# Performance work log

Hardware: AMD Instinct MI355X
Metric: run time of the kernel (lower is better)

The kernel has to match this reference:

```python
import jax, jax.numpy as jnp
import numpy as np

N, E, F_IN, H, C = 50000, 800000, 50, 128, 121


def setup_inputs() -> dict:
    key = jax.random.key(0)
    ks = jax.random.split(key, 16)
    s = 0.05
    inp = {
        'x': jax.random.normal(ks[0], (N, F_IN), jnp.float32),
        'edge_index': jax.random.randint(ks[1], (2, E), 0, N, jnp.int64),
        'TRAIN': 0,
        'W1': jax.random.normal(ks[2], (F_IN, H), jnp.float32) * s,
        'b1': jnp.zeros((H,), jnp.float32),
        'W2': jax.random.normal(ks[3], (H, H), jnp.float32) * s,
        'b2': jnp.zeros((H,), jnp.float32),
        'W3': jax.random.normal(ks[4], (H, H), jnp.float32) * s,
        'b3': jnp.zeros((H,), jnp.float32),
        'fcW1': jax.random.normal(ks[5], (H, H), jnp.float32) * s,
        'fcb1': jnp.zeros((H,), jnp.float32),
        'fcW2': jax.random.normal(ks[6], (H, H), jnp.float32) * s,
        'fcb2': jnp.zeros((H,), jnp.float32),
        'fcW3': jax.random.normal(ks[7], (H, C), jnp.float32) * s,
        'fcb3': jnp.zeros((C,), jnp.float32),
    }
    return inp


def gcn_conv(x, W, b, src, dst, n):
    # PyG GCNConv: h = x @ W; symmetric norm with self-loops; aggregate at dst.
    h = x @ W
    deg = jax.ops.segment_sum(jnp.ones(src.shape[0], h.dtype), dst, num_segments=n) + 1.0
    dinv = jax.lax.rsqrt(deg)  # deg^{-1/2}, self-loop included
    norm = dinv[src] * dinv[dst]  # [E]
    agg = jax.ops.segment_sum(h[src] * norm[:, None], dst, num_segments=n)
    agg = agg + h * (dinv * dinv)[:, None]  # self-loop contribution
    return agg + b


def reference(x, edge_index, TRAIN, W1, b1, W2, b2, W3, b3, fcW1, fcb1, fcW2, fcb2, fcW3, fcb3):
    src, dst = edge_index[0], edge_index[1]
    n = x.shape[0]
    y = jax.nn.relu(gcn_conv(x, W1, b1, src, dst, n))
    y = jax.nn.relu(gcn_conv(y, W2, b2, src, dst, n))
    y = jax.nn.relu(gcn_conv(y, W3, b3, src, dst, n))
    y = jax.nn.relu(y @ fcW1 + fcb1)
    y = jax.nn.relu(y @ fcW2 + fcb2)
    y = y @ fcW3 + fcb3
    return y
```

## Files before the change

### kernel.cpp

```cpp
#include <hip/hip_runtime.h>

#define SCAN_CHUNK 2048

typedef short s16x8 __attribute__((ext_vector_type(8)));
typedef float f32x4 __attribute__((ext_vector_type(4)));

__device__ inline ushort f2b(float f) {
  uint u = __float_as_uint(f);
  return (ushort)((u + 0x7fffu + ((u >> 16) & 1u)) >> 16);
}
__device__ inline float b2f(uint h) { return __uint_as_float(h << 16); }

__global__ __launch_bounds__(256) void convert_hist_kernel(const void* __restrict__ ei,
                                                           int* __restrict__ src,
                                                           int* __restrict__ dst,
                                                           int* __restrict__ degi, int E) {
  __shared__ int sflag;
  if (threadIdx.x == 0) {
    const int* p32 = (const int*)ei;
    int is64 = 1;
#pragma unroll 4
    for (int i = 1; i < 256; i += 2)
      if (p32[i] != 0) { is64 = 0; break; }
    sflag = is64;
  }
  __syncthreads();
  int e = blockIdx.x * 256 + threadIdx.x;
  if (e >= E) return;
  int s, d;
  if (sflag) {
    const long long* p = (const long long*)ei;
    s = (int)p[e];
    d = (int)p[E + e];
  } else {
    const int* p = (const int*)ei;
    s = p[e];
    d = p[E + e];
  }
  src[e] = s;
  dst[e] = d;
  atomicAdd(&degi[d], 1);
}

__global__ __launch_bounds__(256) void chunk_reduce_kernel(const int* __restrict__ degi,
                                                           int* __restrict__ partials, int N) {
  __shared__ int s[256];
  int base = blockIdx.x * SCAN_CHUNK;
  int sum = 0;
  for (int j = 0; j < 8; ++j) {
    int i = base + threadIdx.x * 8 + j;
    if (i < N) sum += degi[i];
  }
  s[threadIdx.x] = sum;
  __syncthreads();
  for (int ofs = 128; ofs > 0; ofs >>= 1) {
    if ((int)threadIdx.x < ofs) s[threadIdx.x] += s[threadIdx.x + ofs];
    __syncthreads();
  }
  if (threadIdx.x == 0) partials[blockIdx.x] = s[0];
}

__global__ __launch_bounds__(256) void chunk_scan_kernel(int* __restrict__ degi,
                                                         const int* __restrict__ partials,
                                                         int nchunk,
                                                         int* __restrict__ rowptr,
                                                         float* __restrict__ dinv,
                                                         int N, int E) {
  __shared__ int s[256];
  __shared__ int sbase;
  int t = threadIdx.x;
  if (t == 0) {
    int acc = 0;
    for (int c = 0; c < (int)blockIdx.x; ++c) acc += partials[c];
    sbase = acc;
    if (blockIdx.x == 0) rowptr[N] = E;
  }
  int base = blockIdx.x * SCAN_CHUNK;
  int v[8];
  int tsum = 0;
  for (int j = 0; j < 8; ++j) {
    int i = base + t * 8 + j;
    v[j] = (i < N) ? degi[i] : 0;
    tsum += v[j];
  }
  s[t] = tsum;
  __syncthreads();
  for (int ofs = 1; ofs < 256; ofs <<= 1) {
    int add = (t >= ofs) ? s[t - ofs] : 0;
    __syncthreads();
    s[t] += add;
    __syncthreads();
  }
  int run = s[t] - tsum + sbase;
  for (int j = 0; j < 8; ++j) {
    int i = base + t * 8 + j;
    if (i < N) {
      rowptr[i] = run;
      dinv[i] = rsqrtf((float)v[j] + 1.0f);
      degi[i] = 0;
    }
    run += v[j];
  }
}

__global__ __launch_bounds__(256) void scatter_kernel(const int* __restrict__ src,
                                                      const int* __restrict__ dst,
                                                      const int* __restrict__ rowptr,
                                                      const float* __restrict__ dinv,
                                                      int* __restrict__ cnt,
                                                      uint* __restrict__ epack, int E, int N) {
  const int chunk = blockIdx.x & 7;
  const int group = blockIdx.x >> 3;
  const int ngroup = gridDim.x >> 3;
  const int c0 = (int)(((long)chunk * N) >> 3);
  const int c1 = (int)(((long)(chunk + 1) * N) >> 3);
  for (int e = group * 256 + threadIdx.x; e < E; e += ngroup * 256) {
    int d = dst[e];
    if (d < c0 || d >= c1) continue;
    int s = src[e];
    int slot = rowptr[d] + atomicAdd(&cnt[d], 1);
    float nm = dinv[s] * dinv[d];
    epack[slot] = (uint)s | ((uint)f2b(nm) << 16);
  }
}

__global__ __launch_bounds__(256) void prep_all(const float* __restrict__ W1,
                                                const float* __restrict__ W2,
                                                const float* __restrict__ W3,
                                                const float* __restrict__ F1,
                                                const float* __restrict__ F2,
                                                const float* __restrict__ F3,
                                                const float* __restrict__ x,
                                                ushort* __restrict__ W1t, ushort* __restrict__ W2t,
                                                ushort* __restrict__ W3t, ushort* __restrict__ F1t,
                                                ushort* __restrict__ F2t, ushort* __restrict__ F3t,
                                                ushort* __restrict__ xb, int N) {
  int b = blockIdx.x;
  if (b < 384) {
    int wi = b >> 6;
    int i = (b & 63) * 256 + threadIdx.x;
    const float* W;
    ushort* Wt;
    int K, Kp, ncol;
    switch (wi) {
      case 0: W = W1; Wt = W1t; K = 50; Kp = 64; ncol = 128; break;
      case 1: W = W2; Wt = W2t; K = 128; Kp = 128; ncol = 128; break;
      case 2: W = W3; Wt = W3t; K = 128; Kp = 128; ncol = 128; break;
      case 3: W = F1; Wt = F1t; K = 128; Kp = 128; ncol = 128; break;
      case 4: W = F2; Wt = F2t; K = 128; Kp = 128; ncol = 128; break;
      default: W = F3; Wt = F3t; K = 128; Kp = 128; ncol = 121; break;
    }
    if (i >= 128 * Kp) return;
    int c = i / Kp, k = i - c * Kp;
    float w = (k < K && c < ncol) ? W[(size_t)k * ncol + c] : 0.f;
    ushort hi = f2b(w);
    float rem = w - b2f(hi);
    Wt[(size_t)c * Kp + k] = hi;
    Wt[(size_t)128 * Kp + (size_t)c * Kp + k] = f2b(rem);
  } else {
    long i = (long)(b - 384) * 256 + threadIdx.x;
    if (i >= (long)N * 64) return;
    int n = (int)(i >> 6), k = (int)(i & 63);
    xb[i] = (k < 50) ? f2b(x[(size_t)n * 50 + k]) : (ushort)0;
  }
}

template <int KSTEPS, bool BIAS, bool RELU>
__global__ __launch_bounds__(256) void mm_mfma(const ushort* __restrict__ X,
                                               const ushort* __restrict__ Wt,
                                               const float* __restrict__ bias,
                                               ushort* __restrict__ Yb, int N) {
  constexpr int K = KSTEPS * 32;
  const int lane = threadIdx.x & 63;
  const int wq = threadIdx.x >> 6;
  const long r0 = (long)blockIdx.x * 32;
  if (r0 >= N) return;
  const bool v1 = (r0 + 16) < N;
  const int am = lane & 15;
  const int ag = lane >> 4;
  const ushort* __restrict__ x0 = X + (size_t)(r0 + am) * K + ag * 8;

  f32x4 acc[2][2] = {};
  for (int ks = 0; ks < KSTEPS; ++ks) {
    s16x8 a0 = *(const s16x8*)(x0 + ks * 32);
    s16x8 a1 = {};
    if (v1) a1 = *(const s16x8*)(x0 + (size_t)16 * K + ks * 32);
#pragma unroll
    for (int f = 0; f < 2; ++f) {
      const ushort* wp = Wt + (size_t)(wq * 32 + f * 16 + am) * K + ag * 8 + ks * 32;
      s16x8 bh = *(const s16x8*)(wp);
      s16x8 bl = *(const s16x8*)(wp + (size_t)128 * K);
      acc[0][f] = __builtin_amdgcn_mfma_f32_16x16x32_bf16(a0, bh, acc[0][f], 0, 0, 0);
      acc[0][f] = __builtin_amdgcn_mfma_f32_16x16x32_bf16(a0, bl, acc[0][f], 0, 0, 0);
      if (v1) {
        acc[1][f] = __builtin_amdgcn_mfma_f32_16x16x32_bf16(a1, bh, acc[1][f], 0, 0, 0);
        acc[1][f] = __builtin_amdgcn_mfma_f32_16x16x32_bf16(a1, bl, acc[1][f], 0, 0, 0);
      }
    }
  }

  const int dr = ag * 4;
#pragma unroll
  for (int m = 0; m < 2; ++m) {
    if (m == 1 && !v1) break;
#pragma unroll
    for (int f = 0; f < 2; ++f) {
      int col = wq * 32 + f * 16 + am;
      float bv = BIAS ? bias[col] : 0.f;
#pragma unroll
      for (int r = 0; r < 4; ++r) {
        long row = r0 + m * 16 + dr + r;
        float v = acc[m][f][r] + bv;
        if (RELU) v = fmaxf(v, 0.f);
        Yb[row * 128 + col] = f2b(v);
      }
    }
  }
}

__global__ __launch_bounds__(256) void fc_fused(const ushort* __restrict__ X,
                                                const ushort* __restrict__ F1t,
                                                const ushort* __restrict__ F2t,
                                                const ushort* __restrict__ F3t,
                                                const float* __restrict__ b1,
                                                const float* __restrict__ b2,
                                                const float* __restrict__ b3,
                                                float* __restrict__ out, int N) {
  __shared__ ushort lds[32 * 128];
  const int lane = threadIdx.x & 63;
  const int wq = threadIdx.x >> 6;
  const long r0 = (long)blockIdx.x * 32;
  if (r0 >= N) return;
  const bool v1 = (r0 + 16) < N;
  const int am = lane & 15;
  const int ag = lane >> 4;
  char* my = (char*)lds;

  auto stage = [&](f32x4 acc[2][2], const float* __restrict__ bias) {
#pragma unroll
    for (int m = 0; m < 2; ++m)
#pragma unroll
      for (int f = 0; f < 2; ++f) {
        int col = wq * 32 + f * 16 + am;
        float bv = bias[col];
#pragma unroll
        for (int r = 0; r < 4; ++r) {
          int row = m * 16 + ag * 4 + r;
          uint byte = (uint)(row * 256 + col * 2) ^ ((uint)(row & 7) << 4);
          *(ushort*)(my + byte) = f2b(fmaxf(acc[m][f][r] + bv, 0.f));
        }
      }
  };
  auto loadA = [&](int m, int ks) -> s16x8 {
    int row = m * 16 + am;
    uint byte = (uint)(row * 256 + ks * 64 + ag * 16) ^ ((uint)(row & 7) << 4);
    return *(const s16x8*)(my + byte);
  };
  auto layer = [&](f32x4 acc[2][2], const ushort* __restrict__ Wt, bool fromLds,
                   const ushort* __restrict__ x0) {
#pragma unroll
    for (int ks = 0; ks < 4; ++ks) {
      s16x8 a0, a1;
      if (fromLds) {
        a0 = loadA(0, ks);
        a1 = loadA(1, ks);
      } else {
        a0 = *(const s16x8*)(x0 + ks * 32);
        a1 = v1 ? *(const s16x8*)(x0 + (size_t)16 * 128 + ks * 32) : s16x8{};
      }
#pragma unroll
      for (int f = 0; f < 2; ++f) {
        const ushort* wp = Wt + (size_t)(wq * 32 + f * 16 + am) * 128 + ag * 8 + ks * 32;
        s16x8 bh = *(const s16x8*)(wp);
        s16x8 bl = *(const s16x8*)(wp + (size_t)128 * 128);
        acc[0][f] = __builtin_amdgcn_mfma_f32_16x16x32_bf16(a0, bh, acc[0][f], 0, 0, 0);
        acc[0][f] = __builtin_amdgcn_mfma_f32_16x16x32_bf16(a0, bl, acc[0][f], 0, 0, 0);
        acc[1][f] = __builtin_amdgcn_mfma_f32_16x16x32_bf16(a1, bh, acc[1][f], 0, 0, 0);
        acc[1][f] = __builtin_amdgcn_mfma_f32_16x16x32_bf16(a1, bl, acc[1][f], 0, 0, 0);
      }
    }
  };

  const ushort* x0 = X + (size_t)(r0 + am) * 128 + ag * 8;
  f32x4 a1c[2][2] = {};
  layer(a1c, F1t, false, x0);
  stage(a1c, b1);
  __syncthreads();
  f32x4 a2c[2][2] = {};
  layer(a2c, F2t, true, nullptr);
  __syncthreads();
  stage(a2c, b2);
  __syncthreads();
  f32x4 a3c[2][2] = {};
  layer(a3c, F3t, true, nullptr);

#pragma unroll
  for (int m = 0; m < 2; ++m) {
    if (m == 1 && !v1) break;
#pragma unroll
    for (int f = 0; f < 2; ++f) {
      int col = wq * 32 + f * 16 + am;
      if (col >= 121) continue;
      float bv = b3[col];
#pragma unroll
      for (int r = 0; r < 4; ++r) {
        long row = r0 + m * 16 + ag * 4 + r;
        if (row < N) out[row * 121 + col] = a3c[m][f][r] + bv;
      }
    }
  }
}

template <int RW, bool ACT>
__global__ __launch_bounds__(256) void agg_kernel(const ushort* __restrict__ Hm,
                                                  const int* __restrict__ rowptr,
                                                  const uint* __restrict__ epack,
                                                  const float* __restrict__ dinv,
                                                  const float* __restrict__ b,
                                                  ushort* __restrict__ Y, int N) {
  int wave = threadIdx.x >> 6;
  int lane = threadIdx.x & 63;
  int n = blockIdx.x * 4 + wave;
  if (n >= N) return;
  int beg = rowptr[n], end = rowptr[n + 1];
  float dn = dinv[n];
  float d2 = dn * dn;
  int i = beg;

  if constexpr (RW == 128) {
    int f = lane * 2;
    float ax = 0.f, ay = 0.f;
    while (i + 8 <= end) {
      uint rec[8];
#pragma unroll
      for (int j = 0; j < 8; ++j) rec[j] = epack[i + j];
      uint v[8];
#pragma unroll
      for (int j = 0; j < 8; ++j)
        v[j] = *(const uint*)&Hm[(size_t)(rec[j] & 0xffffu) * 128 + f];
#pragma unroll
      for (int j = 0; j < 8; ++j) {
        float nm = __uint_as_float(rec[j] & 0xffff0000u);
        ax += b2f(v[j] & 0xffffu) * nm;
        ay += b2f(v[j] >> 16) * nm;
      }
      i += 8;
    }
    if (i + 4 <= end) {
      uint rec[4];
#pragma unroll
      for (int j = 0; j < 4; ++j) rec[j] = epack[i + j];
      uint v[4];
#pragma unroll
      for (int j = 0; j < 4; ++j)
        v[j] = *(const uint*)&Hm[(size_t)(rec[j] & 0xffffu) * 128 + f];
#pragma unroll
      for (int j = 0; j < 4; ++j) {
        float nm = __uint_as_float(rec[j] & 0xffff0000u);
        ax += b2f(v[j] & 0xffffu) * nm;
        ay += b2f(v[j] >> 16) * nm;
      }
      i += 4;
    }
    for (; i < end; ++i) {
      uint rec = epack[i];
      float nm = __uint_as_float(rec & 0xffff0000u);
      uint v = *(const uint*)&Hm[(size_t)(rec & 0xffffu) * 128 + f];
      ax += b2f(v & 0xffffu) * nm;
      ay += b2f(v >> 16) * nm;
    }
    uint sv = *(const uint*)&Hm[(size_t)n * 128 + f];
    ax += b2f(sv & 0xffffu) * d2;
    ay += b2f(sv >> 16) * d2;
    if (ACT) {
      ax = fmaxf(ax + b[f], 0.f);
      ay = fmaxf(ay + b[f + 1], 0.f);
    }
    uint out = (uint)f2b(ax) | ((uint)f2b(ay) << 16);
    *(uint*)&Y[(size_t)n * 128 + f] = out;
  } else {
    int f = lane;
    float ax = 0.f;
    while (i + 8 <= end) {
      uint rec[8];
#pragma unroll
      for (int j = 0; j < 8; ++j) rec[j] = epack[i + j];
      ushort v[8];
#pragma unroll
      for (int j = 0; j < 8; ++j)
        v[j] = Hm[(size_t)(rec[j] & 0xffffu) * 64 + f];
#pragma unroll
      for (int j = 0; j < 8; ++j)
        ax += b2f(v[j]) * __uint_as_float(rec[j] & 0xffff0000u);
      i += 8;
    }
    if (i + 4 <= end) {
      uint rec[4];
#pragma unroll
      for (int j = 0; j < 4; ++j) rec[j] = epack[i + j];
      ushort v[4];
#pragma unroll
      for (int j = 0; j < 4; ++j)
        v[j] = Hm[(size_t)(rec[j] & 0xffffu) * 64 + f];
#pragma unroll
      for (int j = 0; j < 4; ++j)
        ax += b2f(v[j]) * __uint_as_float(rec[j] & 0xffff0000u);
      i += 4;
    }
    for (; i < end; ++i) {
      uint rec = epack[i];
      ax += b2f(Hm[(size_t)(rec & 0xffffu) * 64 + f]) * __uint_as_float(rec & 0xffff0000u);
    }
    ax += b2f(Hm[(size_t)n * 64 + f]) * d2;
    if (ACT) ax = fmaxf(ax + b[f], 0.f);
    Y[(size_t)n * 64 + f] = f2b(ax);
  }
}

extern "C" void kernel_launch(void* const* d_in, const int* in_sizes, int n_in,
                              void* d_out, int out_size, void* d_ws, size_t ws_size,
                              hipStream_t stream) {
  const float* x    = (const float*)d_in[0];
  const void*  ei   = d_in[1];
  const float* W1   = (const float*)d_in[3];
  const float* b1   = (const float*)d_in[4];
  const float* W2   = (const float*)d_in[5];
  const float* b2   = (const float*)d_in[6];
  const float* W3   = (const float*)d_in[7];
  const float* b3   = (const float*)d_in[8];
  const float* fcW1 = (const float*)d_in[9];
  const float* fcb1 = (const float*)d_in[10];
  const float* fcW2 = (const float*)d_in[11];
  const float* fcb2 = (const float*)d_in[12];
  const float* fcW3 = (const float*)d_in[13];
  const float* fcb3 = (const float*)d_in[14];

  const int FIN = 50;
  const int N = in_sizes[0] / FIN;
  const int E = in_sizes[1] / 2;
  const int NCHUNK = (N + SCAN_CHUNK - 1) / SCAN_CHUNK;

  size_t off = 0;
  auto carve = [&](size_t bytes) {
    void* p = (char*)d_ws + off;
    off += (bytes + 255) & ~(size_t)255;
    return p;
  };
  int*    src32    = (int*)carve((size_t)E * 4);
  int*    dst32    = (int*)carve((size_t)E * 4);
  uint*   epack    = (uint*)carve((size_t)E * 4);
  int*    degi     = (int*)carve((size_t)N * 4);
  int*    rowptr   = (int*)carve((size_t)(N + 1) * 4);
  float*  dinv     = (float*)carve((size_t)N * 4);
  int*    partials = (int*)carve((size_t)NCHUNK * 4);
  ushort* W1t      = (ushort*)carve((size_t)2 * 128 * 64 * 2);
  ushort* W2t      = (ushort*)carve((size_t)2 * 128 * 128 * 2);
  ushort* W3t      = (ushort*)carve((size_t)2 * 128 * 128 * 2);
  ushort* F1t      = (ushort*)carve((size_t)2 * 128 * 128 * 2);
  ushort* F2t      = (ushort*)carve((size_t)2 * 128 * 128 * 2);
  ushort* F3t      = (ushort*)carve((size_t)2 * 128 * 128 * 2);
  ushort* xb       = (ushort*)carve((size_t)N * 64 * 2);
  ushort* aggX     = (ushort*)carve((size_t)N * 64 * 2);
  ushort* bufA     = (ushort*)carve((size_t)N * 128 * 2);
  ushort* bufB     = (ushort*)carve((size_t)N * 128 * 2);

  const int gE = (E + 255) / 256;
  const int gMM = (N + 31) / 32;
  const int gAGG = (N + 3) / 4;
  const int gPREP = 384 + (int)(((long)N * 64 + 255) / 256);

  hipMemsetAsync(degi, 0, (size_t)N * 4, stream);
  convert_hist_kernel<<<gE, 256, 0, stream>>>(ei, src32, dst32, degi, E);
  chunk_reduce_kernel<<<NCHUNK, 256, 0, stream>>>(degi, partials, N);
  chunk_scan_kernel<<<NCHUNK, 256, 0, stream>>>(degi, partials, NCHUNK, rowptr, dinv, N, E);
  scatter_kernel<<<1024, 256, 0, stream>>>(src32, dst32, rowptr, dinv, degi, epack, E, N);
  prep_all<<<gPREP, 256, 0, stream>>>(W1, W2, W3, fcW1, fcW2, fcW3, x,
                                      W1t, W2t, W3t, F1t, F2t, F3t, xb, N);

  agg_kernel<64, false><<<gAGG, 256, 0, stream>>>(xb, rowptr, epack, dinv, nullptr, aggX, N);
  mm_mfma<2, true, true><<<gMM, 256, 0, stream>>>(aggX, W1t, b1, bufA, N);
  mm_mfma<4, false, false><<<gMM, 256, 0, stream>>>(bufA, W2t, nullptr, bufB, N);
  agg_kernel<128, true><<<gAGG, 256, 0, stream>>>(bufB, rowptr, epack, dinv, b2, bufA, N);
  mm_mfma<4, false, false><<<gMM, 256, 0, stream>>>(bufA, W3t, nullptr, bufB, N);
  agg_kernel<128, true><<<gAGG, 256, 0, stream>>>(bufB, rowptr, epack, dinv, b3, bufA, N);
  fc_fused<<<gMM, 256, 0, stream>>>(bufA, F1t, F2t, F3t, fcb1, fcb2, fcb3,
                                    (float*)d_out, N);
}
```

Baseline: 307.2 us.

## Drop split-bf16 weights, keep weights in registers with persistent grid-stride GEMM tiles

Weights are now stored as a single bf16 copy instead of a hi/lo split, which halves the MFMA count and weight loads in every dense layer. The mm and fused-FC kernels load their weight fragments and biases into registers once and then loop over row tiles with a fixed grid of 1024 blocks, so per-tile weight refetches go away. The trade-off is lower weight precision, a possible accuracy drift against the fp32 reference, and much higher register pressure in fc_fused, which holds three weight sets at once.

```diff
diff --git a/kernel.cpp b/kernel.cpp
--- a/kernel.cpp
+++ b/kernel.cpp
@@ -153,10 +153,7 @@
     if (i >= 128 * Kp) return;
     int c = i / Kp, k = i - c * Kp;
     float w = (k < K && c < ncol) ? W[(size_t)k * ncol + c] : 0.f;
-    ushort hi = f2b(w);
-    float rem = w - b2f(hi);
-    Wt[(size_t)c * Kp + k] = hi;
-    Wt[(size_t)128 * Kp + (size_t)c * Kp + k] = f2b(rem);
+    Wt[(size_t)c * Kp + k] = f2b(w);
   } else {
     long i = (long)(b - 384) * 256 + threadIdx.x;
     if (i >= (long)N * 64) return;
@@ -173,46 +170,52 @@
   constexpr int K = KSTEPS * 32;
   const int lane = threadIdx.x & 63;
   const int wq = threadIdx.x >> 6;
-  const long r0 = (long)blockIdx.x * 32;
-  if (r0 >= N) return;
-  const bool v1 = (r0 + 16) < N;
   const int am = lane & 15;
   const int ag = lane >> 4;
-  const ushort* __restrict__ x0 = X + (size_t)(r0 + am) * K + ag * 8;
-
-  f32x4 acc[2][2] = {};
-  for (int ks = 0; ks < KSTEPS; ++ks) {
-    s16x8 a0 = *(const s16x8*)(x0 + ks * 32);
-    s16x8 a1 = {};
-    if (v1) a1 = *(const s16x8*)(x0 + (size_t)16 * K + ks * 32);
-#pragma unroll
-    for (int f = 0; f < 2; ++f) {
-      const ushort* wp = Wt + (size_t)(wq * 32 + f * 16 + am) * K + ag * 8 + ks * 32;
-      s16x8 bh = *(const s16x8*)(wp);
-      s16x8 bl = *(const s16x8*)(wp + (size_t)128 * K);
-      acc[0][f] = __builtin_amdgcn_mfma_f32_16x16x32_bf16(a0, bh, acc[0][f], 0, 0, 0);
-      acc[0][f] = __builtin_amdgcn_mfma_f32_16x16x32_bf16(a0, bl, acc[0][f], 0, 0, 0);
-      if (v1) {
-        acc[1][f] = __builtin_amdgcn_mfma_f32_16x16x32_bf16(a1, bh, acc[1][f], 0, 0, 0);
-        acc[1][f] = __builtin_amdgcn_mfma_f32_16x16x32_bf16(a1, bl, acc[1][f], 0, 0, 0);
-      }
-    }
-  }
-
-  const int dr = ag * 4;
-#pragma unroll
-  for (int m = 0; m < 2; ++m) {
-    if (m == 1 && !v1) break;
-#pragma unroll
-    for (int f = 0; f < 2; ++f) {
-      int col = wq * 32 + f * 16 + am;
-      float bv = BIAS ? bias[col] : 0.f;
-#pragma unroll
-      for (int r = 0; r < 4; ++r) {
-        long row = r0 + m * 16 + dr + r;
-        float v = acc[m][f][r] + bv;
-        if (RELU) v = fmaxf(v, 0.f);
-        Yb[row * 128 + col] = f2b(v);
+
+  s16x8 wf[KSTEPS][2];
+#pragma unroll
+  for (int ks = 0; ks < KSTEPS; ++ks)
+#pragma unroll
+    for (int f = 0; f < 2; ++f)
+      wf[ks][f] = *(const s16x8*)(Wt + (size_t)(wq * 32 + f * 16 + am) * K + ag * 8 + ks * 32);
+  float bv[2] = {0.f, 0.f};
+  if (BIAS) {
+    bv[0] = bias[wq * 32 + am];
+    bv[1] = bias[wq * 32 + 16 + am];
+  }
+
+  const int ntile = (N + 31) >> 5;
+  for (int t = blockIdx.x; t < ntile; t += gridDim.x) {
+    const long r0 = (long)t * 32;
+    const bool v1 = (r0 + 16) < N;
+    const ushort* x0 = X + (size_t)(r0 + am) * K + ag * 8;
+    f32x4 acc[2][2] = {};
+#pragma unroll
+    for (int ks = 0; ks < KSTEPS; ++ks) {
+      s16x8 a0 = *(const s16x8*)(x0 + ks * 32);
+      s16x8 a1 = {};
+      if (v1) a1 = *(const s16x8*)(x0 + (size_t)16 * K + ks * 32);
+#pragma unroll
+      for (int f = 0; f < 2; ++f) {
+        acc[0][f] = __builtin_amdgcn_mfma_f32_16x16x32_bf16(a0, wf[ks][f], acc[0][f], 0, 0, 0);
+        if (v1)
+          acc[1][f] = __builtin_amdgcn_mfma_f32_16x16x32_bf16(a1, wf[ks][f], acc[1][f], 0, 0, 0);
+      }
+    }
+#pragma unroll
+    for (int m = 0; m < 2; ++m) {
+      if (m == 1 && !v1) break;
+#pragma unroll
+      for (int f = 0; f < 2; ++f) {
+        int col = wq * 32 + f * 16 + am;
+#pragma unroll
+        for (int r = 0; r < 4; ++r) {
+          long row = r0 + m * 16 + ag * 4 + r;
+          float v = acc[m][f][r] + bv[f];
+          if (RELU) v = fmaxf(v, 0.f);
+          Yb[row * 128 + col] = f2b(v);
+        }
       }
     }
   }
@@ -229,25 +232,36 @@
   __shared__ ushort lds[32 * 128];
   const int lane = threadIdx.x & 63;
   const int wq = threadIdx.x >> 6;
-  const long r0 = (long)blockIdx.x * 32;
-  if (r0 >= N) return;
-  const bool v1 = (r0 + 16) < N;
   const int am = lane & 15;
   const int ag = lane >> 4;
   char* my = (char*)lds;
 
-  auto stage = [&](f32x4 acc[2][2], const float* __restrict__ bias) {
+  s16x8 wf1[4][2], wf2[4][2], wf3[4][2];
+#pragma unroll
+  for (int ks = 0; ks < 4; ++ks)
+#pragma unroll
+    for (int f = 0; f < 2; ++f) {
+      size_t o = (size_t)(wq * 32 + f * 16 + am) * 128 + ag * 8 + ks * 32;
+      wf1[ks][f] = *(const s16x8*)(F1t + o);
+      wf2[ks][f] = *(const s16x8*)(F2t + o);
+      wf3[ks][f] = *(const s16x8*)(F3t + o);
+    }
+  float b1v[2] = {b1[wq * 32 + am], b1[wq * 32 + 16 + am]};
+  float b2v[2] = {b2[wq * 32 + am], b2[wq * 32 + 16 + am]};
+  int c0 = wq * 32 + am, c1 = wq * 32 + 16 + am;
+  float b3v[2] = {(c0 < 121) ? b3[c0] : 0.f, (c1 < 121) ? b3[c1] : 0.f};
+
+  auto stage = [&](f32x4 acc[2][2], const float* bv) {
 #pragma unroll
     for (int m = 0; m < 2; ++m)
 #pragma unroll
       for (int f = 0; f < 2; ++f) {
         int col = wq * 32 + f * 16 + am;
-        float bv = bias[col];
 #pragma unroll
         for (int r = 0; r < 4; ++r) {
           int row = m * 16 + ag * 4 + r;
           uint byte = (uint)(row * 256 + col * 2) ^ ((uint)(row & 7) << 4);
-          *(ushort*)(my + byte) = f2b(fmaxf(acc[m][f][r] + bv, 0.f));
+          *(ushort*)(my + byte) = f2b(fmaxf(acc[m][f][r] + bv[f], 0.f));
         }
       }
   };
@@ -256,58 +270,66 @@
     uint byte = (uint)(row * 256 + ks * 64 + ag * 16) ^ ((uint)(row & 7) << 4);
     return *(const s16x8*)(my + byte);
   };
-  auto layer = [&](f32x4 acc[2][2], const ushort* __restrict__ Wt, bool fromLds,
-                   const ushort* __restrict__ x0) {
+
+  const int ntile = (N + 31) >> 5;
+  for (int t = blockIdx.x; t < ntile; t += gridDim.x) {
+    const long r0 = (long)t * 32;
+    const bool v1 = (r0 + 16) < N;
+    const ushort* x0 = X + (size_t)(r0 + am) * 128 + ag * 8;
+
+    f32x4 a1c[2][2] = {};
 #pragma unroll
     for (int ks = 0; ks < 4; ++ks) {
-      s16x8 a0, a1;
-      if (fromLds) {
-        a0 = loadA(0, ks);
-        a1 = loadA(1, ks);
-      } else {
-        a0 = *(const s16x8*)(x0 + ks * 32);
-        a1 = v1 ? *(const s16x8*)(x0 + (size_t)16 * 128 + ks * 32) : s16x8{};
-      }
-#pragma unroll
-      for (int f = 0; f < 2; ++f) {
-        const ushort* wp = Wt + (size_t)(wq * 32 + f * 16 + am) * 128 + ag * 8 + ks * 32;
-        s16x8 bh = *(const s16x8*)(wp);
-        s16x8 bl = *(const s16x8*)(wp + (size_t)128 * 128);
-        acc[0][f] = __builtin_amdgcn_mfma_f32_16x16x32_bf16(a0, bh, acc[0][f], 0, 0, 0);
-        acc[0][f] = __builtin_amdgcn_mfma_f32_16x16x32_bf16(a0, bl, acc[0][f], 0, 0, 0);
-        acc[1][f] = __builtin_amdgcn_mfma_f32_16x16x32_bf16(a1, bh, acc[1][f], 0, 0, 0);
-        acc[1][f] = __builtin_amdgcn_mfma_f32_16x16x32_bf16(a1, bl, acc[1][f], 0, 0, 0);
-      }
-    }
-  };
-
-  const ushort* x0 = X + (size_t)(r0 + am) * 128 + ag * 8;
-  f32x4 a1c[2][2] = {};
-  layer(a1c, F1t, false, x0);
-  stage(a1c, b1);
-  __syncthreads();
-  f32x4 a2c[2][2] = {};
-  layer(a2c, F2t, true, nullptr);
-  __syncthreads();
-  stage(a2c, b2);
-  __syncthreads();
-  f32x4 a3c[2][2] = {};
-  layer(a3c, F3t, true, nullptr);
-
-#pragma unroll
-  for (int m = 0; m < 2; ++m) {
-    if (m == 1 && !v1) break;
-#pragma unroll
-    for (int f = 0; f < 2; ++f) {
-      int col = wq * 32 + f * 16 + am;
-      if (col >= 121) continue;
-      float bv = b3[col];
-#pragma unroll
-      for (int r = 0; r < 4; ++r) {
-        long row = r0 + m * 16 + ag * 4 + r;
-        if (row < N) out[row * 121 + col] = a3c[m][f][r] + bv;
-      }
-    }
+      s16x8 a0 = *(const s16x8*)(x0 + ks * 32);
+      s16x8 a1 = v1 ? *(const s16x8*)(x0 + (size_t)16 * 128 + ks * 32) : s16x8{};
+#pragma unroll
+      for (int f = 0; f < 2; ++f) {
+        a1c[0][f] = __builtin_amdgcn_mfma_f32_16x16x32_bf16(a0, wf1[ks][f], a1c[0][f], 0, 0, 0);
+        a1c[1][f] = __builtin_amdgcn_mfma_f32_16x16x32_bf16(a1, wf1[ks][f], a1c[1][f], 0, 0, 0);
+      }
+    }
+    stage(a1c, b1v);
+    __syncthreads();
+    f32x4 a2c[2][2] = {};
+#pragma unroll
+    for (int ks = 0; ks < 4; ++ks) {
+      s16x8 a0 = loadA(0, ks);
+      s16x8 a1 = loadA(1, ks);
+#pragma unroll
+      for (int f = 0; f < 2; ++f) {
+        a2c[0][f] = __builtin_amdgcn_mfma_f32_16x16x32_bf16(a0, wf2[ks][f], a2c[0][f], 0, 0, 0);
+        a2c[1][f] = __builtin_amdgcn_mfma_f32_16x16x32_bf16(a1, wf2[ks][f], a2c[1][f], 0, 0, 0);
+      }
+    }
+    __syncthreads();
+    stage(a2c, b2v);
+    __syncthreads();
+    f32x4 a3c[2][2] = {};
+#pragma unroll
+    for (int ks = 0; ks < 4; ++ks) {
+      s16x8 a0 = loadA(0, ks);
+      s16x8 a1 = loadA(1, ks);
+#pragma unroll
+      for (int f = 0; f < 2; ++f) {
+        a3c[0][f] = __builtin_amdgcn_mfma_f32_16x16x32_bf16(a0, wf3[ks][f], a3c[0][f], 0, 0, 0);
+        a3c[1][f] = __builtin_amdgcn_mfma_f32_16x16x32_bf16(a1, wf3[ks][f], a3c[1][f], 0, 0, 0);
+      }
+    }
+#pragma unroll
+    for (int m = 0; m < 2; ++m) {
+      if (m == 1 && !v1) break;
+#pragma unroll
+      for (int f = 0; f < 2; ++f) {
+        int col = wq * 32 + f * 16 + am;
+        if (col >= 121) continue;
+#pragma unroll
+        for (int r = 0; r < 4; ++r) {
+          long row = r0 + m * 16 + ag * 4 + r;
+          out[row * 121 + col] = a3c[m][f][r] + b3v[f];
+        }
+      }
+    }
+    __syncthreads();
   }
 }
 
@@ -453,19 +475,19 @@
   int*    rowptr   = (int*)carve((size_t)(N + 1) * 4);
   float*  dinv     = (float*)carve((size_t)N * 4);
   int*    partials = (int*)carve((size_t)NCHUNK * 4);
-  ushort* W1t      = (ushort*)carve((size_t)2 * 128 * 64 * 2);
-  ushort* W2t      = (ushort*)carve((size_t)2 * 128 * 128 * 2);
-  ushort* W3t      = (ushort*)carve((size_t)2 * 128 * 128 * 2);
-  ushort* F1t      = (ushort*)carve((size_t)2 * 128 * 128 * 2);
-  ushort* F2t      = (ushort*)carve((size_t)2 * 128 * 128 * 2);
-  ushort* F3t      = (ushort*)carve((size_t)2 * 128 * 128 * 2);
+  ushort* W1t      = (ushort*)carve((size_t)128 * 64 * 2);
+  ushort* W2t      = (ushort*)carve((size_t)128 * 128 * 2);
+  ushort* W3t      = (ushort*)carve((size_t)128 * 128 * 2);
+  ushort* F1t      = (ushort*)carve((size_t)128 * 128 * 2);
+  ushort* F2t      = (ushort*)carve((size_t)128 * 128 * 2);
+  ushort* F3t      = (ushort*)carve((size_t)128 * 128 * 2);
   ushort* xb       = (ushort*)carve((size_t)N * 64 * 2);
   ushort* aggX     = (ushort*)carve((size_t)N * 64 * 2);
   ushort* bufA     = (ushort*)carve((size_t)N * 128 * 2);
   ushort* bufB     = (ushort*)carve((size_t)N * 128 * 2);
 
   const int gE = (E + 255) / 256;
-  const int gMM = (N + 31) / 32;
+  const int gMM = 1024;
   const int gAGG = (N + 3) / 4;
   const int gPREP = 384 + (int)(((long)N * 64 + 255) / 256);
 
```

Measured after the change: 259.8 us. -15.4%, faster.
